# Performance work log

Measured on AMD Instinct MI355X. Metric: run time of the kernel, lower is better.

The kernel has to match this reference:

```python
import jax, jax.numpy as jnp
import numpy as np

BN_EPS = 1e-5
DIST_EPS = 1e-8


def setup_inputs() -> dict:
    key = jax.random.key(0)
    ks = jax.random.split(key, 8)
    B, N, M = 8, 8192, 2048
    C1, C2 = 128, 256
    Cin = C1 + C2  # 384
    H = 256
    return {
        "xyz1": jax.random.normal(ks[0], (B, N, 3), dtype=jnp.float32),
        "xyz2": jax.random.normal(ks[1], (B, M, 3), dtype=jnp.float32),
        "points1": jax.random.normal(ks[2], (B, N, C1), dtype=jnp.float32),
        "points2": jax.random.normal(ks[3], (B, M, C2), dtype=jnp.float32),
        "W1": jax.random.normal(ks[4], (H, Cin), dtype=jnp.float32) * 0.05,
        "b1": jnp.zeros((H,), dtype=jnp.float32),
        "gamma1": jnp.ones((H,), dtype=jnp.float32),
        "beta1": jnp.zeros((H,), dtype=jnp.float32),
        "W2": jax.random.normal(ks[5], (H, H), dtype=jnp.float32) * 0.05,
        "b2": jnp.zeros((H,), dtype=jnp.float32),
        "gamma2": jnp.ones((H,), dtype=jnp.float32),
        "beta2": jnp.zeros((H,), dtype=jnp.float32),
    }


def _interpolate(xyz1, xyz2, points2):
    # squared distances (B,N,M) via the bmm expansion, as in square_distance
    d = (jnp.sum(xyz1 * xyz1, -1)[:, :, None]
         + jnp.sum(xyz2 * xyz2, -1)[:, None, :]
         - 2.0 * jnp.einsum("bnc,bmc->bnm", xyz1, xyz2))
    neg, idx = jax.lax.top_k(-d, 3)          # 3 smallest distances
    dists = -neg                              # (B,N,3)
    recip = 1.0 / (dists + DIST_EPS)
    w = recip / jnp.sum(recip, -1, keepdims=True)  # (B,N,3)
    gathered = jax.vmap(lambda p, i: p[i])(points2, idx)  # (B,N,3,C2)
    return jnp.einsum("bnkc,bnk->bnc", gathered, w)


def _conv_bn_relu(x, W, b, gamma, beta):
    # pointwise conv1d: (B,N,Cin) x (Cout,Cin) -> (B,N,Cout)
    y = jnp.einsum("bnc,oc->bno", x, W) + b
    mean = jnp.mean(y, axis=(0, 1))           # BatchNorm1d (training-mode batch stats)
    var = jnp.var(y, axis=(0, 1))
    y = (y - mean) * jax.lax.rsqrt(var + BN_EPS) * gamma + beta
    return jax.nn.relu(y)


def reference(xyz1, xyz2, points1, points2, W1, b1, gamma1, beta1, W2, b2, gamma2, beta2):
    interp = _interpolate(xyz1, xyz2, points2)          # (B,N,C2)
    x = jnp.concatenate([points1, interp], axis=-1)     # (B,N,C1+C2)
    x = _conv_bn_relu(x, W1, b1, gamma1, beta1)
    x = _conv_bn_relu(x, W2, b2, gamma2, beta2)
    return x  # (B,N,mlp[-1])
```

## Files before the change

### kernel.cpp

```cpp
#include <hip/hip_runtime.h>
#include <hip/hip_bf16.h>
#include <stdint.h>

#define B_SZ  8
#define N_Q   8192
#define M_PT  2048
#define C1    128
#define C2    256
#define CIN   384
#define H_OUT 256
#define R_TOT 65536

#define NCH   8
#define CHM   (M_PT / NCH)

typedef __bf16 bf16x8 __attribute__((ext_vector_type(8)));
typedef __bf16 bf16x4 __attribute__((ext_vector_type(4)));
typedef float  f32x4  __attribute__((ext_vector_type(4)));

__device__ __forceinline__ void async_copy16(const void* g, void* l) {
    __builtin_amdgcn_global_load_lds(
        (const __attribute__((address_space(1))) unsigned int*)g,
        (__attribute__((address_space(3))) unsigned int*)l,
        16, 0, 0);
}

__global__ __launch_bounds__(256) void knn_vals(
    const float* __restrict__ xyz1, const float* __restrict__ xyz2,
    const float* __restrict__ p2,   const float* __restrict__ W1,
    const float* __restrict__ W2,
    __bf16* __restrict__ p2b,  __bf16* __restrict__ wb1a,
    __bf16* __restrict__ wb1b, __bf16* __restrict__ wb2,
    float4* __restrict__ vals4) {
    __shared__ float4 pos[CHM];
    const int tid = threadIdx.x;
    const int c   = blockIdx.x & (NCH - 1);
    const int qb  = (blockIdx.x >> 3) & 31;
    const int b   = blockIdx.x >> 8;
    const int gid = blockIdx.x * 256 + tid;

    {
        const float4* src = (const float4*)p2 + (size_t)gid * 2;
        float4 a = src[0], bb = src[1];
        bf16x8 o;
        o[0]=(__bf16)a.x; o[1]=(__bf16)a.y; o[2]=(__bf16)a.z; o[3]=(__bf16)a.w;
        o[4]=(__bf16)bb.x; o[5]=(__bf16)bb.y; o[6]=(__bf16)bb.z; o[7]=(__bf16)bb.w;
        *(bf16x8*)(p2b + (size_t)gid * 8) = o;
    }
    if (blockIdx.x < 384) {
        const int e = gid;
        const int o = e / 384, k = e - o * 384;
        __bf16 v = (__bf16)W1[e];
        if (k < C1) wb1a[o * C1 + k] = v;
        else        wb1b[o * C2 + (k - C1)] = v;
    } else if (blockIdx.x < 640) {
        const int e = gid - 98304;
        wb2[e] = (__bf16)W2[e];
    }

    {
        const float* x2 = xyz2 + ((size_t)b * M_PT + c * CHM) * 3;
        float x = x2[tid * 3], y = x2[tid * 3 + 1], z = x2[tid * 3 + 2];
        pos[tid] = make_float4(-2.f * x, -2.f * y, -2.f * z,
                               fmaf(x, x, fmaf(y, y, z * z)));
    }
    __syncthreads();

    const int q = b * N_Q + qb * 256 + tid;
    const float* q1 = xyz1 + (size_t)q * 3;
    float x1 = q1[0], y1 = q1[1], z1 = q1[2];
    float v0 = 3.4e38f, v1 = 3.4e38f, v2 = 3.4e38f;
#pragma unroll 8
    for (int j = 0; j < CHM; ++j) {
        float4 p = pos[j];
        float d  = fmaf(p.x, x1, fmaf(p.y, y1, fmaf(p.z, z1, p.w)));
        float n0 = fminf(d, v0);
        float n1 = __builtin_amdgcn_fmed3f(d, v0, v1);
        float n2 = __builtin_amdgcn_fmed3f(d, v1, v2);
        v0 = n0; v1 = n1; v2 = n2;
    }
    vals4[(size_t)c * R_TOT + q] = make_float4(v0, v1, v2, 0.f);
}

__global__ __launch_bounds__(256) void knn_recover(
    const float* __restrict__ xyz1, const float* __restrict__ xyz2,
    const float* __restrict__ p1,   const float4* __restrict__ vals4,
    __bf16* __restrict__ p1b, float4* __restrict__ w4,
    int4* __restrict__ ci4) {
    __shared__ float4 pos[CHM];
    const int tid = threadIdx.x;
    const int c   = blockIdx.x & (NCH - 1);
    const int qb  = (blockIdx.x >> 3) & 31;
    const int b   = blockIdx.x >> 8;
    const int gid = blockIdx.x * 256 + tid;

    {
        const float4* src = (const float4*)p1 + (size_t)gid * 4;
        float4 a = src[0], bb = src[1], cc = src[2], dd = src[3];
        bf16x8 o0, o1;
        o0[0]=(__bf16)a.x; o0[1]=(__bf16)a.y; o0[2]=(__bf16)a.z; o0[3]=(__bf16)a.w;
        o0[4]=(__bf16)bb.x; o0[5]=(__bf16)bb.y; o0[6]=(__bf16)bb.z; o0[7]=(__bf16)bb.w;
        o1[0]=(__bf16)cc.x; o1[1]=(__bf16)cc.y; o1[2]=(__bf16)cc.z; o1[3]=(__bf16)cc.w;
        o1[4]=(__bf16)dd.x; o1[5]=(__bf16)dd.y; o1[6]=(__bf16)dd.z; o1[7]=(__bf16)dd.w;
        *(bf16x8*)(p1b + (size_t)gid * 16)     = o0;
        *(bf16x8*)(p1b + (size_t)gid * 16 + 8) = o1;
    }

    {
        const float* x2 = xyz2 + ((size_t)b * M_PT + c * CHM) * 3;
        float x = x2[tid * 3], y = x2[tid * 3 + 1], z = x2[tid * 3 + 2];
        pos[tid] = make_float4(-2.f * x, -2.f * y, -2.f * z,
                               fmaf(x, x, fmaf(y, y, z * z)));
    }
    __syncthreads();

    const int q = b * N_Q + qb * 256 + tid;
    const float* q1 = xyz1 + (size_t)q * 3;
    float x1 = q1[0], y1 = q1[1], z1 = q1[2];

    float v0 = 3.4e38f, v1 = 3.4e38f, v2 = 3.4e38f;
#pragma unroll
    for (int cc = 0; cc < NCH; ++cc) {
        float4 t = vals4[(size_t)cc * R_TOT + q];
#pragma unroll
        for (int k = 0; k < 3; ++k) {
            float d  = (k == 0) ? t.x : (k == 1) ? t.y : t.z;
            float n0 = fminf(d, v0);
            float n1 = __builtin_amdgcn_fmed3f(d, v0, v1);
            float n2 = __builtin_amdgcn_fmed3f(d, v1, v2);
            v0 = n0; v1 = n1; v2 = n2;
        }
    }
    if (c == 0) {
        float n1q = fmaf(x1, x1, fmaf(y1, y1, z1 * z1));
        float r0 = 1.f / ((v0 + n1q) + 1e-8f);
        float r1 = 1.f / ((v1 + n1q) + 1e-8f);
        float r2 = 1.f / ((v2 + n1q) + 1e-8f);
        float rs = 1.f / (r0 + r1 + r2);
        w4[q] = make_float4(r0 * rs, r1 * rs, r2 * rs, 0.f);
    }

    int i0 = 0x7fffffff, i1 = 0x7fffffff, i2 = 0x7fffffff;
    const int jb = c * CHM;
#pragma unroll 4
    for (int j = 0; j < CHM; ++j) {
        float4 p = pos[j];
        float d  = fmaf(p.x, x1, fmaf(p.y, y1, fmaf(p.z, z1, p.w)));
        if (d <= v2) {
            const int jj = jb + j;
            i0 = min(i0, (d == v0) ? jj : 0x7fffffff);
            i1 = min(i1, (d == v1) ? jj : 0x7fffffff);
            i2 = min(i2, (d == v2) ? jj : 0x7fffffff);
        }
    }
    ci4[(size_t)c * R_TOT + q] = make_int4(i0, i1, i2, 0);
}

template <int K, bool STATS>
__global__ __launch_bounds__(256, 2) void gemm_bt(const __bf16* __restrict__ A,
                                                  const __bf16* __restrict__ Bw,
                                                  __bf16* __restrict__ Cout,
                                                  float* __restrict__ partS,
                                                  float* __restrict__ partQ) {
    __shared__ __attribute__((aligned(16))) __bf16 As[128 * 32];
    __shared__ __attribute__((aligned(16))) __bf16 Bs[128 * 32];
    const int tid  = threadIdx.x;
    const int wave = tid >> 6, lane = tid & 63;
    const int wm = wave >> 1, wn = wave & 1;
    const int quad = lane >> 4, r16 = lane & 15;
    const int bx = blockIdx.x & 1, by = blockIdx.x >> 1;
    const int l4 = lane >> 2, lk = (lane & 3) * 8;

    f32x4 acc[4][4] = {};

    const __bf16* gA = A  + (size_t)(by * 128 + wave * 32 + l4) * K + lk;
    const __bf16* gB = Bw + (size_t)(bx * 128 + wave * 32 + l4) * K + lk;
    char* lA = (char*)As + wave * 2048;
    char* lB = (char*)Bs + wave * 2048;

    for (int k0 = 0; k0 < K; k0 += 32) {
        async_copy16(gA + k0,                  lA);
        async_copy16(gA + k0 + (size_t)16 * K, lA + 1024);
        async_copy16(gB + k0,                  lB);
        async_copy16(gB + k0 + (size_t)16 * K, lB + 1024);
        __syncthreads();

        bf16x8 af[4], bf[4];
#pragma unroll
        for (int t = 0; t < 4; ++t)
            af[t] = *(const bf16x8*)(As + (wm * 64 + t * 16 + r16) * 32 + quad * 8);
#pragma unroll
        for (int u = 0; u < 4; ++u)
            bf[u] = *(const bf16x8*)(Bs + (wn * 64 + u * 16 + r16) * 32 + quad * 8);
#pragma unroll
        for (int t = 0; t < 4; ++t)
#pragma unroll
            for (int u = 0; u < 4; ++u)
                acc[t][u] = __builtin_amdgcn_mfma_f32_16x16x32_bf16(af[t], bf[u], acc[t][u], 0, 0, 0);
        __syncthreads();
    }

#pragma unroll
    for (int t = 0; t < 4; ++t) {
#pragma unroll
        for (int u = 0; u < 4; ++u) {
            const int col = bx * 128 + wn * 64 + u * 16 + r16;
#pragma unroll
            for (int r = 0; r < 4; ++r) {
                const int row = by * 128 + wm * 64 + t * 16 + quad * 4 + r;
                Cout[(size_t)row * H_OUT + col] = (__bf16)acc[t][u][r];
            }
        }
    }

    if constexpr (STATS) {
        float* redS = (float*)As;
        float* redQ = ((float*)As) + 1024;
        const int slot = wm * 4 + quad;
#pragma unroll
        for (int u = 0; u < 4; ++u) {
            float s = 0.f, qq = 0.f;
#pragma unroll
            for (int t = 0; t < 4; ++t)
#pragma unroll
                for (int r = 0; r < 4; ++r) { float v = acc[t][u][r]; s += v; qq = fmaf(v, v, qq); }
            const int col = wn * 64 + u * 16 + r16;
            redS[col * 8 + slot] = s;
            redQ[col * 8 + slot] = qq;
        }
        __syncthreads();
        if (tid < 128) {
            float s = 0.f, qq = 0.f;
#pragma unroll
            for (int k = 0; k < 8; ++k) { s += redS[tid * 8 + k]; qq += redQ[tid * 8 + k]; }
            partS[(size_t)blockIdx.x * 128 + tid] = s;
            partQ[(size_t)blockIdx.x * 128 + tid] = qq;
        }
    }
}

__global__ __launch_bounds__(256, 2) void gemm_a_int(
    const __bf16* __restrict__ A,  const __bf16* __restrict__ Bw,
    const __bf16* __restrict__ zb, const int4* __restrict__ ci4,
    const float4* __restrict__ w4, __bf16* __restrict__ Cout,
    float* __restrict__ partS, float* __restrict__ partQ) {
    constexpr int K = C1;
    __shared__ __attribute__((aligned(16))) __bf16 As[128 * 32];
    __shared__ __attribute__((aligned(16))) __bf16 Bs[128 * 32];
    const int tid  = threadIdx.x;
    const int wave = tid >> 6, lane = tid & 63;
    const int wm = wave >> 1, wn = wave & 1;
    const int quad = lane >> 4, r16 = lane & 15;
    const int bx = blockIdx.x & 1, by = blockIdx.x >> 1;
    const int l4 = lane >> 2, lk = (lane & 3) * 8;

    f32x4 acc[4][4] = {};

    const __bf16* gA = A  + (size_t)(by * 128 + wave * 32 + l4) * K + lk;
    const __bf16* gB = Bw + (size_t)(bx * 128 + wave * 32 + l4) * K + lk;
    char* lA = (char*)As + wave * 2048;
    char* lB = (char*)Bs + wave * 2048;

    for (int k0 = 0; k0 < K; k0 += 32) {
        async_copy16(gA + k0,                  lA);
        async_copy16(gA + k0 + (size_t)16 * K, lA + 1024);
        async_copy16(gB + k0,                  lB);
        async_copy16(gB + k0 + (size_t)16 * K, lB + 1024);
        __syncthreads();

        bf16x8 af[4], bf[4];
#pragma unroll
        for (int t = 0; t < 4; ++t)
            af[t] = *(const bf16x8*)(As + (wm * 64 + t * 16 + r16) * 32 + quad * 8);
#pragma unroll
        for (int u = 0; u < 4; ++u)
            bf[u] = *(const bf16x8*)(Bs + (wn * 64 + u * 16 + r16) * 32 + quad * 8);
#pragma unroll
        for (int t = 0; t < 4; ++t)
#pragma unroll
            for (int u = 0; u < 4; ++u)
                acc[t][u] = __builtin_amdgcn_mfma_f32_16x16x32_bf16(af[t], bf[u], acc[t][u], 0, 0, 0);
        __syncthreads();
    }

    if (tid < 128) {
        const int q = by * 128 + tid;
        int i0 = 0x7fffffff, i1 = 0x7fffffff, i2 = 0x7fffffff;
#pragma unroll
        for (int cc = 0; cc < NCH; ++cc) {
            int4 t4 = ci4[(size_t)cc * R_TOT + q];
            i0 = min(i0, t4.x); i1 = min(i1, t4.y); i2 = min(i2, t4.z);
        }
        float4 w = w4[q];
        ((int4*)As)[tid * 2]       = make_int4(i0, i1, i2, 0);
        ((float4*)As)[tid * 2 + 1] = make_float4(w.x, w.y, w.z, 0.f);
    }
    __syncthreads();

    const int bbase = (by >> 6) * M_PT;
#pragma unroll
    for (int t = 0; t < 4; ++t) {
#pragma unroll
        for (int r = 0; r < 4; ++r) {
            const int rl = wm * 64 + t * 16 + quad * 4 + r;
            const int4   ii = ((const int4*)As)[rl * 2];
            const float4 ww = ((const float4*)As)[rl * 2 + 1];
            const __bf16* z0 = zb + (size_t)(bbase + ii.x) * H_OUT;
            const __bf16* z1 = zb + (size_t)(bbase + ii.y) * H_OUT;
            const __bf16* z2 = zb + (size_t)(bbase + ii.z) * H_OUT;
#pragma unroll
            for (int u = 0; u < 4; ++u) {
                const int col = bx * 128 + wn * 64 + u * 16 + r16;
                acc[t][u][r] += ww.x * (float)z0[col] + ww.y * (float)z1[col]
                              + ww.z * (float)z2[col];
            }
        }
    }

#pragma unroll
    for (int t = 0; t < 4; ++t) {
#pragma unroll
        for (int u = 0; u < 4; ++u) {
            const int col = bx * 128 + wn * 64 + u * 16 + r16;
#pragma unroll
            for (int r = 0; r < 4; ++r) {
                const int row = by * 128 + wm * 64 + t * 16 + quad * 4 + r;
                Cout[(size_t)row * H_OUT + col] = (__bf16)acc[t][u][r];
            }
        }
    }

    __syncthreads();
    float* redS = (float*)As;
    float* redQ = ((float*)As) + 1024;
    const int slot = wm * 4 + quad;
#pragma unroll
    for (int u = 0; u < 4; ++u) {
        float s = 0.f, qq = 0.f;
#pragma unroll
        for (int t = 0; t < 4; ++t)
#pragma unroll
            for (int r = 0; r < 4; ++r) { float v = acc[t][u][r]; s += v; qq = fmaf(v, v, qq); }
        const int col = wn * 64 + u * 16 + r16;
        redS[col * 8 + slot] = s;
        redQ[col * 8 + slot] = qq;
    }
    __syncthreads();
    if (tid < 128) {
        float s = 0.f, qq = 0.f;
#pragma unroll
        for (int k = 0; k < 8; ++k) { s += redS[tid * 8 + k]; qq += redQ[tid * 8 + k]; }
        partS[(size_t)blockIdx.x * 128 + tid] = s;
        partQ[(size_t)blockIdx.x * 128 + tid] = qq;
    }
}

__global__ __launch_bounds__(256) void bn_finalize(const float* __restrict__ pS,
                                                   const float* __restrict__ pQ,
                                                   const float* __restrict__ gamma,
                                                   const float* __restrict__ beta,
                                                   float* __restrict__ sc,
                                                   float* __restrict__ sh) {
    __shared__ float rs[256], rq[256];
    const int c = blockIdx.x;
    const int t = threadIdx.x;
    const int half = c >> 7, lo = c & 127;
    const size_t o1 = (size_t)(2 * t + half) * 128 + lo;
    const size_t o2 = (size_t)(2 * (t + 256) + half) * 128 + lo;
    rs[t] = pS[o1] + pS[o2];
    rq[t] = pQ[o1] + pQ[o2];
    __syncthreads();
    for (int k = 128; k > 0; k >>= 1) {
        if (t < k) { rs[t] += rs[t + k]; rq[t] += rq[t + k]; }
        __syncthreads();
    }
    if (t == 0) {
        const float inv = 1.f / (float)R_TOT;
        float mean = rs[0] * inv;
        float var  = rq[0] * inv - mean * mean;
        float a    = gamma[c] * rsqrtf(var + 1e-5f);
        sc[c] = a;
        sh[c] = beta[c] - mean * a;
    }
}

__global__ __launch_bounds__(256) void apply_bf16(__bf16* __restrict__ y,
                                                  const float* __restrict__ sc,
                                                  const float* __restrict__ sh) {
    __shared__ float scs[256], shs[256];
    scs[threadIdx.x] = sc[threadIdx.x];
    shs[threadIdx.x] = sh[threadIdx.x];
    __syncthreads();
    size_t i = ((size_t)blockIdx.x * 256 + threadIdx.x) * 8;
    int c0 = (int)(i & 255);
    bf16x8 v = *(const bf16x8*)(y + i);
#pragma unroll
    for (int e = 0; e < 8; ++e) {
        float f = fmaf((float)v[e], scs[c0 + e], shs[c0 + e]);
        v[e] = (__bf16)fmaxf(f, 0.f);
    }
    *(bf16x8*)(y + i) = v;
}

__global__ __launch_bounds__(256) void apply_out(const __bf16* __restrict__ y,
                                                 const float* __restrict__ sc,
                                                 const float* __restrict__ sh,
                                                 float* __restrict__ out) {
    __shared__ float scs[256], shs[256];
    scs[threadIdx.x] = sc[threadIdx.x];
    shs[threadIdx.x] = sh[threadIdx.x];
    __syncthreads();
    size_t i = ((size_t)blockIdx.x * 256 + threadIdx.x) * 8;
    int c0 = (int)(i & 255);
    bf16x8 v = *(const bf16x8*)(y + i);
    f32x4 o0, o1;
#pragma unroll
    for (int e = 0; e < 4; ++e)
        o0[e] = fmaxf(fmaf((float)v[e], scs[c0 + e], shs[c0 + e]), 0.f);
#pragma unroll
    for (int e = 0; e < 4; ++e)
        o1[e] = fmaxf(fmaf((float)v[4 + e], scs[c0 + 4 + e], shs[c0 + 4 + e]), 0.f);
    *(f32x4*)(out + i)     = o0;
    *(f32x4*)(out + i + 4) = o1;
}

extern "C" void kernel_launch(void* const* d_in, const int* in_sizes, int n_in,
                              void* d_out, int out_size, void* d_ws, size_t ws_size,
                              hipStream_t stream) {
    const float* xyz1 = (const float*)d_in[0];
    const float* xyz2 = (const float*)d_in[1];
    const float* p1   = (const float*)d_in[2];
    const float* p2   = (const float*)d_in[3];
    const float* W1   = (const float*)d_in[4];
    const float* g1   = (const float*)d_in[6];
    const float* be1  = (const float*)d_in[7];
    const float* W2   = (const float*)d_in[8];
    const float* g2   = (const float*)d_in[10];
    const float* be2  = (const float*)d_in[11];
    float* out = (float*)d_out;

    char* ws = (char*)d_ws;
    __bf16* y1b   = (__bf16*)(ws);
    int4*   ci4   = (int4*)  (ws + 33554432);
    float4* vals4 = (float4*)(ws + 41943040);
    __bf16* zb    = (__bf16*)(ws + 41943040);
    float4* w4    = (float4*)(ws + 50331648);
    __bf16* p2b   = (__bf16*)(ws + 51380224);
    __bf16* p1b   = (__bf16*)(ws + 59768832);
    __bf16* y2b   = (__bf16*)(ws + 33554432);
    __bf16* wb1a  = (__bf16*)(ws + 76546048);
    __bf16* wb1b  = (__bf16*)(ws + 76611584);
    __bf16* wb2   = (__bf16*)(ws + 76742656);
    float*  sc1   = (float*) (ws + 76873728);
    float*  sh1   = sc1 + 256;
    float*  sc2   = sc1 + 512;
    float*  sh2   = sc1 + 768;

    float* partS1 = (float*)d_out;
    float* partQ1 = partS1 + 131072;
    float* partS2 = partS1 + 262144;
    float* partQ2 = partS1 + 393216;

    knn_vals<<<2048, 256, 0, stream>>>(xyz1, xyz2, p2, W1, W2,
                                       p2b, wb1a, wb1b, wb2, vals4);
    knn_recover<<<2048, 256, 0, stream>>>(xyz1, xyz2, p1, vals4, p1b, w4, ci4);

    gemm_bt<C2, false><<<256, 256, 0, stream>>>(p2b, wb1b, zb, nullptr, nullptr);
    gemm_a_int<<<1024, 256, 0, stream>>>(p1b, wb1a, zb, ci4, w4, y1b,
                                         partS1, partQ1);
    bn_finalize<<<256, 256, 0, stream>>>(partS1, partQ1, g1, be1, sc1, sh1);
    apply_bf16<<<8192, 256, 0, stream>>>(y1b, sc1, sh1);

    gemm_bt<H_OUT, true><<<1024, 256, 0, stream>>>(y1b, wb2, y2b, partS2, partQ2);
    bn_finalize<<<256, 256, 0, stream>>>(partS2, partQ2, g2, be2, sc2, sh2);
    apply_out<<<8192, 256, 0, stream>>>(y2b, sc2, sh2, out);
}
```

Baseline: 261.8 us.

## Replace brute-force KNN with x-sorted sweep and early termination

The brute-force chunked 3-NN search (two passes over all 2048 reference points per query, plus an index-recovery pass) is replaced by a rank sort of xyz2 along x, followed by a bidirectional sweep from each query's binary-searched position. The sweep stops once the squared x-gap exceeds the current third-best distance. Two lanes per query scan opposite directions and merge their results at the end, which removes the partial-result buffers and the index reduction in the GEMM. Sweep length now depends on the data and causes wave divergence, and the fixed iteration cap and tolerance-based stopping test could affect exactness at ties or boundaries.

```diff
diff --git a/kernel.cpp b/kernel.cpp
--- a/kernel.cpp
+++ b/kernel.cpp
@@ -11,9 +11,6 @@
 #define H_OUT 256
 #define R_TOT 65536
 
-#define NCH   8
-#define CHM   (M_PT / NCH)
-
 typedef __bf16 bf16x8 __attribute__((ext_vector_type(8)));
 typedef __bf16 bf16x4 __attribute__((ext_vector_type(4)));
 typedef float  f32x4  __attribute__((ext_vector_type(4)));
@@ -25,19 +22,42 @@
         16, 0, 0);
 }
 
-__global__ __launch_bounds__(256) void knn_vals(
-    const float* __restrict__ xyz1, const float* __restrict__ xyz2,
+__global__ __launch_bounds__(256) void convert_sort(
+    const float* __restrict__ xyz2, const float* __restrict__ p1,
     const float* __restrict__ p2,   const float* __restrict__ W1,
     const float* __restrict__ W2,
-    __bf16* __restrict__ p2b,  __bf16* __restrict__ wb1a,
-    __bf16* __restrict__ wb1b, __bf16* __restrict__ wb2,
-    float4* __restrict__ vals4) {
-    __shared__ float4 pos[CHM];
+    __bf16* __restrict__ p1b,  __bf16* __restrict__ p2b,
+    __bf16* __restrict__ wb1a, __bf16* __restrict__ wb1b,
+    __bf16* __restrict__ wb2,  float4* __restrict__ sorted) {
     const int tid = threadIdx.x;
-    const int c   = blockIdx.x & (NCH - 1);
-    const int qb  = (blockIdx.x >> 3) & 31;
-    const int b   = blockIdx.x >> 8;
-    const int gid = blockIdx.x * 256 + tid;
+
+    if (blockIdx.x < 64) {
+        __shared__ __attribute__((aligned(16))) float xs[M_PT];
+        const int b  = blockIdx.x >> 3;
+        const int ch = blockIdx.x & 7;
+        const float* x2 = xyz2 + (size_t)b * M_PT * 3;
+#pragma unroll
+        for (int j = tid; j < M_PT; j += 256) xs[j] = x2[j * 3];
+        __syncthreads();
+        const int   i  = ch * 256 + tid;
+        const float xi = xs[i];
+        const float yi = x2[i * 3 + 1], zi = x2[i * 3 + 2];
+        int rank = 0;
+#pragma unroll 4
+        for (int j = 0; j < M_PT; j += 4) {
+            const float4 xv = *(const float4*)&xs[j];
+            rank += (xv.x < xi || (xv.x == xi && (j + 0) < i)) ? 1 : 0;
+            rank += (xv.y < xi || (xv.y == xi && (j + 1) < i)) ? 1 : 0;
+            rank += (xv.z < xi || (xv.z == xi && (j + 2) < i)) ? 1 : 0;
+            rank += (xv.w < xi || (xv.w == xi && (j + 3) < i)) ? 1 : 0;
+        }
+        sorted[(size_t)b * M_PT + rank] =
+            make_float4(xi, yi, zi, __int_as_float(i));
+        return;
+    }
+
+    const int cb  = blockIdx.x - 64;
+    const int gid = cb * 256 + tid;
 
     {
         const float4* src = (const float4*)p2 + (size_t)gid * 2;
@@ -47,53 +67,16 @@
         o[4]=(__bf16)bb.x; o[5]=(__bf16)bb.y; o[6]=(__bf16)bb.z; o[7]=(__bf16)bb.w;
         *(bf16x8*)(p2b + (size_t)gid * 8) = o;
     }
-    if (blockIdx.x < 384) {
+    if (cb < 384) {
         const int e = gid;
         const int o = e / 384, k = e - o * 384;
         __bf16 v = (__bf16)W1[e];
         if (k < C1) wb1a[o * C1 + k] = v;
         else        wb1b[o * C2 + (k - C1)] = v;
-    } else if (blockIdx.x < 640) {
+    } else if (cb < 640) {
         const int e = gid - 98304;
         wb2[e] = (__bf16)W2[e];
     }
-
-    {
-        const float* x2 = xyz2 + ((size_t)b * M_PT + c * CHM) * 3;
-        float x = x2[tid * 3], y = x2[tid * 3 + 1], z = x2[tid * 3 + 2];
-        pos[tid] = make_float4(-2.f * x, -2.f * y, -2.f * z,
-                               fmaf(x, x, fmaf(y, y, z * z)));
-    }
-    __syncthreads();
-
-    const int q = b * N_Q + qb * 256 + tid;
-    const float* q1 = xyz1 + (size_t)q * 3;
-    float x1 = q1[0], y1 = q1[1], z1 = q1[2];
-    float v0 = 3.4e38f, v1 = 3.4e38f, v2 = 3.4e38f;
-#pragma unroll 8
-    for (int j = 0; j < CHM; ++j) {
-        float4 p = pos[j];
-        float d  = fmaf(p.x, x1, fmaf(p.y, y1, fmaf(p.z, z1, p.w)));
-        float n0 = fminf(d, v0);
-        float n1 = __builtin_amdgcn_fmed3f(d, v0, v1);
-        float n2 = __builtin_amdgcn_fmed3f(d, v1, v2);
-        v0 = n0; v1 = n1; v2 = n2;
-    }
-    vals4[(size_t)c * R_TOT + q] = make_float4(v0, v1, v2, 0.f);
-}
-
-__global__ __launch_bounds__(256) void knn_recover(
-    const float* __restrict__ xyz1, const float* __restrict__ xyz2,
-    const float* __restrict__ p1,   const float4* __restrict__ vals4,
-    __bf16* __restrict__ p1b, float4* __restrict__ w4,
-    int4* __restrict__ ci4) {
-    __shared__ float4 pos[CHM];
-    const int tid = threadIdx.x;
-    const int c   = blockIdx.x & (NCH - 1);
-    const int qb  = (blockIdx.x >> 3) & 31;
-    const int b   = blockIdx.x >> 8;
-    const int gid = blockIdx.x * 256 + tid;
-
     {
         const float4* src = (const float4*)p1 + (size_t)gid * 4;
         float4 a = src[0], bb = src[1], cc = src[2], dd = src[3];
@@ -105,55 +88,108 @@
         *(bf16x8*)(p1b + (size_t)gid * 16)     = o0;
         *(bf16x8*)(p1b + (size_t)gid * 16 + 8) = o1;
     }
+}
+
+__global__ __launch_bounds__(256, 4) void knn_sweep(
+    const float* __restrict__ xyz1, const float4* __restrict__ sorted,
+    float4* __restrict__ w4, int4* __restrict__ gidx4) {
+    __shared__ __attribute__((aligned(16))) float4 pts[M_PT];
+    const int tid  = threadIdx.x;
+    const int b    = blockIdx.x >> 6;
+    const int qb   = blockIdx.x & 63;
+    const int wave = tid >> 6, lane = tid & 63;
 
     {
-        const float* x2 = xyz2 + ((size_t)b * M_PT + c * CHM) * 3;
-        float x = x2[tid * 3], y = x2[tid * 3 + 1], z = x2[tid * 3 + 2];
-        pos[tid] = make_float4(-2.f * x, -2.f * y, -2.f * z,
-                               fmaf(x, x, fmaf(y, y, z * z)));
-    }
-    __syncthreads();
-
-    const int q = b * N_Q + qb * 256 + tid;
-    const float* q1 = xyz1 + (size_t)q * 3;
-    float x1 = q1[0], y1 = q1[1], z1 = q1[2];
+        const float4* src = sorted + (size_t)b * M_PT;
+#pragma unroll
+        for (int j = 0; j < 8; ++j)
+            async_copy16(src + j * 256 + wave * 64 + lane,
+                         (char*)pts + ((j * 256 + wave * 64) << 4));
+    }
+    __syncthreads();
+
+    const int   side = tid & 1;
+    const int   qid  = b * N_Q + qb * 128 + (tid >> 1);
+    const float* qp  = xyz1 + (size_t)qid * 3;
+    const float qx = qp[0], qy = qp[1], qz = qp[2];
+    const float n1q = fmaf(qx, qx, fmaf(qy, qy, qz * qz));
+
+    int lo = 0, hi = M_PT;
+#pragma unroll
+    for (int s = 0; s < 11; ++s) {
+        const int mid = (lo + hi) >> 1;
+        const bool lt = pts[mid].x < qx;
+        lo = lt ? mid + 1 : lo;
+        hi = lt ? hi : mid;
+    }
 
     float v0 = 3.4e38f, v1 = 3.4e38f, v2 = 3.4e38f;
-#pragma unroll
-    for (int cc = 0; cc < NCH; ++cc) {
-        float4 t = vals4[(size_t)cc * R_TOT + q];
-#pragma unroll
-        for (int k = 0; k < 3; ++k) {
-            float d  = (k == 0) ? t.x : (k == 1) ? t.y : t.z;
-            float n0 = fminf(d, v0);
-            float n1 = __builtin_amdgcn_fmed3f(d, v0, v1);
-            float n2 = __builtin_amdgcn_fmed3f(d, v1, v2);
+    int   i0 = 0, i1 = 0, i2 = 0;
+    int   ptr  = side ? lo : lo - 1;
+    const int step = side ? 1 : -1;
+    bool done = false;
+
+    for (int it = 0; it < 272; ++it) {
+        if (!__any(!done)) break;
+        float lastb = 3.4e38f;
+#pragma unroll
+        for (int k = 0; k < 8; ++k) {
+            const int  pc  = ptr & (M_PT - 1);
+            const bool inb = (unsigned)ptr < (unsigned)M_PT;
+            const float4 p = pts[pc];
+            const float dx = qx - p.x;
+            const float bx = dx * dx;
+            const float pw = fmaf(p.x, p.x, fmaf(p.y, p.y, p.z * p.z));
+            float d = fmaf(-2.f * p.x, qx,
+                      fmaf(-2.f * p.y, qy, fmaf(-2.f * p.z, qz, pw)));
+            d = inb ? d : 3.4e38f;
+            const int j = inb ? __float_as_int(p.w) : 0x7fffffff;
+            const bool c0 = d < v0 || (d == v0 && j < i0);
+            const bool c1 = d < v1 || (d == v1 && j < i1);
+            const bool c2 = d < v2 || (d == v2 && j < i2);
+            const float n0 = fminf(d, v0);
+            const float n1 = __builtin_amdgcn_fmed3f(d, v0, v1);
+            const float n2 = __builtin_amdgcn_fmed3f(d, v1, v2);
+            i2 = c1 ? i1 : (c2 ? j : i2);
+            i1 = c0 ? i0 : (c1 ? j : i1);
+            i0 = c0 ? j  : i0;
             v0 = n0; v1 = n1; v2 = n2;
-        }
-    }
-    if (c == 0) {
-        float n1q = fmaf(x1, x1, fmaf(y1, y1, z1 * z1));
-        float r0 = 1.f / ((v0 + n1q) + 1e-8f);
-        float r1 = 1.f / ((v1 + n1q) + 1e-8f);
-        float r2 = 1.f / ((v2 + n1q) + 1e-8f);
-        float rs = 1.f / (r0 + r1 + r2);
-        w4[q] = make_float4(r0 * rs, r1 * rs, r2 * rs, 0.f);
-    }
-
-    int i0 = 0x7fffffff, i1 = 0x7fffffff, i2 = 0x7fffffff;
-    const int jb = c * CHM;
-#pragma unroll 4
-    for (int j = 0; j < CHM; ++j) {
-        float4 p = pos[j];
-        float d  = fmaf(p.x, x1, fmaf(p.y, y1, fmaf(p.z, z1, p.w)));
-        if (d <= v2) {
-            const int jj = jb + j;
-            i0 = min(i0, (d == v0) ? jj : 0x7fffffff);
-            i1 = min(i1, (d == v1) ? jj : 0x7fffffff);
-            i2 = min(i2, (d == v2) ? jj : 0x7fffffff);
-        }
-    }
-    ci4[(size_t)c * R_TOT + q] = make_int4(i0, i1, i2, 0);
+            if (k == 7) lastb = inb ? bx : 3.4e38f;
+            ptr += step;
+        }
+        const float v2m = fminf(v2, __shfl_xor(v2, 1));
+        const float thr = fminf(v2m + n1q + 1e-3f, 3.0e38f);
+        done = done || (lastb >= thr);
+    }
+
+    const float m0 = __shfl_xor(v0, 1), m1 = __shfl_xor(v1, 1),
+                m2 = __shfl_xor(v2, 1);
+    const int   j0 = __shfl_xor(i0, 1), j1 = __shfl_xor(i1, 1),
+                j2 = __shfl_xor(i2, 1);
+#pragma unroll
+    for (int t = 0; t < 3; ++t) {
+        const float d = (t == 0) ? m0 : (t == 1) ? m1 : m2;
+        const int   j = (t == 0) ? j0 : (t == 1) ? j1 : j2;
+        const bool c0 = d < v0 || (d == v0 && j < i0);
+        const bool c1 = d < v1 || (d == v1 && j < i1);
+        const bool c2 = d < v2 || (d == v2 && j < i2);
+        const float n0 = fminf(d, v0);
+        const float n1 = __builtin_amdgcn_fmed3f(d, v0, v1);
+        const float n2 = __builtin_amdgcn_fmed3f(d, v1, v2);
+        i2 = c1 ? i1 : (c2 ? j : i2);
+        i1 = c0 ? i0 : (c1 ? j : i1);
+        i0 = c0 ? j  : i0;
+        v0 = n0; v1 = n1; v2 = n2;
+    }
+
+    if (side == 0) {
+        const float r0 = 1.f / ((v0 + n1q) + 1e-8f);
+        const float r1 = 1.f / ((v1 + n1q) + 1e-8f);
+        const float r2 = 1.f / ((v2 + n1q) + 1e-8f);
+        const float rs = 1.f / (r0 + r1 + r2);
+        w4[qid]    = make_float4(r0 * rs, r1 * rs, r2 * rs, 0.f);
+        gidx4[qid] = make_int4(i0, i1, i2, 0);
+    }
 }
 
 template <int K, bool STATS>
@@ -241,7 +277,7 @@
 
 __global__ __launch_bounds__(256, 2) void gemm_a_int(
     const __bf16* __restrict__ A,  const __bf16* __restrict__ Bw,
-    const __bf16* __restrict__ zb, const int4* __restrict__ ci4,
+    const __bf16* __restrict__ zb, const int4* __restrict__ gidx4,
     const float4* __restrict__ w4, __bf16* __restrict__ Cout,
     float* __restrict__ partS, float* __restrict__ partQ) {
     constexpr int K = C1;
@@ -285,15 +321,8 @@
 
     if (tid < 128) {
         const int q = by * 128 + tid;
-        int i0 = 0x7fffffff, i1 = 0x7fffffff, i2 = 0x7fffffff;
-#pragma unroll
-        for (int cc = 0; cc < NCH; ++cc) {
-            int4 t4 = ci4[(size_t)cc * R_TOT + q];
-            i0 = min(i0, t4.x); i1 = min(i1, t4.y); i2 = min(i2, t4.z);
-        }
-        float4 w = w4[q];
-        ((int4*)As)[tid * 2]       = make_int4(i0, i1, i2, 0);
-        ((float4*)As)[tid * 2 + 1] = make_float4(w.x, w.y, w.z, 0.f);
+        ((int4*)As)[tid * 2]       = gidx4[q];
+        ((float4*)As)[tid * 2 + 1] = w4[q];
     }
     __syncthreads();
 
@@ -441,8 +470,8 @@
 
     char* ws = (char*)d_ws;
     __bf16* y1b   = (__bf16*)(ws);
-    int4*   ci4   = (int4*)  (ws + 33554432);
-    float4* vals4 = (float4*)(ws + 41943040);
+    int4*   gidx4 = (int4*)  (ws + 33554432);
+    float4* sorted= (float4*)(ws + 34603008);
     __bf16* zb    = (__bf16*)(ws + 41943040);
     float4* w4    = (float4*)(ws + 50331648);
     __bf16* p2b   = (__bf16*)(ws + 51380224);
@@ -461,12 +490,12 @@
     float* partS2 = partS1 + 262144;
     float* partQ2 = partS1 + 393216;
 
-    knn_vals<<<2048, 256, 0, stream>>>(xyz1, xyz2, p2, W1, W2,
-                                       p2b, wb1a, wb1b, wb2, vals4);
-    knn_recover<<<2048, 256, 0, stream>>>(xyz1, xyz2, p1, vals4, p1b, w4, ci4);
+    convert_sort<<<2112, 256, 0, stream>>>(xyz2, p1, p2, W1, W2,
+                                           p1b, p2b, wb1a, wb1b, wb2, sorted);
+    knn_sweep<<<512, 256, 0, stream>>>(xyz1, sorted, w4, gidx4);
 
     gemm_bt<C2, false><<<256, 256, 0, stream>>>(p2b, wb1b, zb, nullptr, nullptr);
-    gemm_a_int<<<1024, 256, 0, stream>>>(p1b, wb1a, zb, ci4, w4, y1b,
+    gemm_a_int<<<1024, 256, 0, stream>>>(p1b, wb1a, zb, gidx4, w4, y1b,
                                          partS1, partQ1);
     bn_finalize<<<256, 256, 0, stream>>>(partS1, partQ1, g1, be1, sc1, sh1);
     apply_bf16<<<8192, 256, 0, stream>>>(y1b, sc1, sh1);
```

Measured after the change: 510.5 us. 95.0% more time.
